# Kernel tuning notes

Hardware: AMD Instinct MI355X
Metric: run time of the kernel (lower is better)

## Reference

```python
import jax, jax.numpy as jnp
import numpy as np

MARGIN = 0.5          # triplet_margin
CLS_W = 1.0           # classification_weight
TRI_W = 1.0           # triplet_weight
SMOOTH = 0.1          # CrossEntropyLoss label_smoothing
PD_EPS = 1e-6         # torch pairwise_distance eps inside TripletMarginLoss


def setup_inputs() -> dict:
    key = jax.random.key(0)
    k1, k2, k3 = jax.random.split(key, 3)
    B, D, C = 8192, 128, 1000
    logits = jax.random.normal(k1, (B, C), dtype=jnp.float32)
    emb = jax.random.normal(k2, (B, D), dtype=jnp.float32)
    emb = emb / jnp.linalg.norm(emb, axis=1, keepdims=True)  # L2-normalized per docstring
    labels = jax.random.randint(k3, (B,), 0, C, dtype=jnp.int32)
    return {"logits": logits, "embeddings": emb, "labels": labels}


def _combined_loss(logits, embeddings, labels):
    # --- cross entropy with label smoothing 0.1 ---
    logp = jax.nn.log_softmax(logits, axis=-1)
    nll = -jnp.take_along_axis(logp, labels[:, None], axis=-1)[:, 0]
    smooth_term = -logp.mean(axis=-1)  # eps/C * sum(-logp) == eps * mean(-logp)
    cls_loss = ((1.0 - SMOOTH) * nll + SMOOTH * smooth_term).mean()

    # --- batch-hard triplet mining (vectorized over all rows) ---
    B = embeddings.shape[0]
    sq = jnp.sum(embeddings * embeddings, axis=1)
    # squared pairwise distances [B,B]; monotone in true distance, so ranking matches cdist
    d2 = sq[:, None] + sq[None, :] - 2.0 * (embeddings @ embeddings.T)
    eq = labels[:, None] == labels[None, :]
    pos_mask = eq & ~jnp.eye(B, dtype=bool)   # same class, not self
    neg_mask = ~eq
    big = jnp.finfo(d2.dtype).max
    hardest_pos = jnp.argmax(jnp.where(pos_mask, d2, -big), axis=1)  # farthest positive
    hardest_neg = jnp.argmin(jnp.where(neg_mask, d2, big), axis=1)   # closest negative
    valid = pos_mask.any(axis=1) & neg_mask.any(axis=1)

    # --- TripletMarginLoss(margin, p=2) over valid triplets ---
    a = embeddings
    p = embeddings[hardest_pos]
    n = embeddings[hardest_neg]
    d_ap = jnp.linalg.norm(a - p + PD_EPS, axis=1)  # torch adds eps inside the norm
    d_an = jnp.linalg.norm(a - n + PD_EPS, axis=1)
    per_row = jnp.maximum(d_ap - d_an + MARGIN, 0.0)
    cnt = jnp.sum(valid)
    triplet_loss = jnp.where(
        cnt > 0,
        jnp.sum(jnp.where(valid, per_row, 0.0)) / jnp.maximum(cnt, 1).astype(per_row.dtype),
        jnp.zeros((), per_row.dtype),
    )

    return CLS_W * cls_loss + TRI_W * triplet_loss


def reference(logits, embeddings, labels):
    return _combined_loss(logits, embeddings, labels)
```

## Files before the change

kernel.cpp:

```cpp
#include <hip/hip_runtime.h>

#define NB 8192
#define ND 128
#define NC 1000
#define NJC 16
#define JCB 4
#define JBS 128
#define NIS 32
#define CAP 64

typedef __attribute__((ext_vector_type(8))) short bf16x8;
typedef __attribute__((ext_vector_type(4))) float f32x4;

__device__ __forceinline__ unsigned short f2bf(float f) {
    unsigned int u = __float_as_uint(f);
    return (unsigned short)((u + 0x7fffu + ((u >> 16) & 1u)) >> 16);
}

__global__ __launch_bounds__(256) void ce_prep_kernel(const float* __restrict__ logits,
                                                      const float* __restrict__ emb,
                                                      const int* __restrict__ labels,
                                                      unsigned short* __restrict__ ebf,
                                                      float* __restrict__ cls_part,
                                                      int* __restrict__ cnt) {
    int wave = threadIdx.x >> 6, lane = threadIdx.x & 63;
    int r = blockIdx.x * 4 + wave;

    if (blockIdx.x == 0) {
        for (int k = threadIdx.x; k < NC; k += 256) cnt[k] = 0;
    }

    {
        const float* erow = emb + (size_t)r * ND;
        float2 v = *(const float2*)(erow + lane * 2);
        unsigned int packed = (unsigned int)f2bf(v.x) | ((unsigned int)f2bf(v.y) << 16);
        *(unsigned int*)(ebf + (size_t)r * ND + lane * 2) = packed;
    }

    const float* x = logits + (size_t)r * NC;
    float4 q0 = *(const float4*)(x + 4 * lane);
    float4 q1 = *(const float4*)(x + 256 + 4 * lane);
    float4 q2 = *(const float4*)(x + 512 + 4 * lane);
    float4 q3;
    bool a3 = (192 + lane) < 250;
    if (a3) q3 = *(const float4*)(x + 768 + 4 * lane);
    else q3 = make_float4(-3.4e38f, -3.4e38f, -3.4e38f, -3.4e38f);

    float m = fmaxf(fmaxf(fmaxf(q0.x, q0.y), fmaxf(q0.z, q0.w)),
                    fmaxf(fmaxf(q1.x, q1.y), fmaxf(q1.z, q1.w)));
    m = fmaxf(m, fmaxf(fmaxf(q2.x, q2.y), fmaxf(q2.z, q2.w)));
    m = fmaxf(m, fmaxf(fmaxf(q3.x, q3.y), fmaxf(q3.z, q3.w)));
    float s = (q0.x + q0.y + q0.z + q0.w) + (q1.x + q1.y + q1.z + q1.w) +
              (q2.x + q2.y + q2.z + q2.w) +
              (a3 ? (q3.x + q3.y + q3.z + q3.w) : 0.f);
#pragma unroll
    for (int o = 32; o >= 1; o >>= 1) {
        m = fmaxf(m, __shfl_xor(m, o));
        s += __shfl_xor(s, o);
    }
    float se = expf(q0.x - m) + expf(q0.y - m) + expf(q0.z - m) + expf(q0.w - m) +
               expf(q1.x - m) + expf(q1.y - m) + expf(q1.z - m) + expf(q1.w - m) +
               expf(q2.x - m) + expf(q2.y - m) + expf(q2.z - m) + expf(q2.w - m) +
               expf(q3.x - m) + expf(q3.y - m) + expf(q3.z - m) + expf(q3.w - m);
#pragma unroll
    for (int o = 32; o >= 1; o >>= 1) se += __shfl_xor(se, o);
    float xl = x[labels[r]];
    float v = (m + logf(se)) - 0.9f * xl - 0.1f * (s * (1.0f / NC));
    if (lane == 0) cls_part[r] = v;
}

__global__ __launch_bounds__(256) void bucket_kernel(const int* __restrict__ labels,
                                                     int* __restrict__ cnt,
                                                     int* __restrict__ lists) {
    int r = blockIdx.x * 256 + threadIdx.x;
    int c = labels[r];
    int slot = atomicAdd(&cnt[c], 1);
    if (slot < CAP) lists[c * CAP + slot] = r;
}

__global__ __launch_bounds__(256, 2) void mine_kernel(const unsigned short* __restrict__ ebf,
                                                      const int* __restrict__ labels,
                                                      float* __restrict__ part) {
    __shared__ unsigned short btile[2][JBS * ND];
    int tid = threadIdx.x;
    int wave = tid >> 6, lane = tid & 63;
    int col = lane & 15, grp = lane >> 4;
    int jchunk = blockIdx.x, jcbase = jchunk * (JCB * JBS);
    int ibase = blockIdx.y * 256 + wave * 64;

#define STAGE(buf, jb0)                                                                \
    do {                                                                               \
        _Pragma("unroll")                                                              \
        for (int rep = 0; rep < 8; ++rep) {                                            \
            int row = (tid >> 4) + rep * 16;                                           \
            const unsigned short* src =                                                \
                ebf + (size_t)((jb0) + row) * ND + (((tid & 15) ^ (row & 7)) << 3);    \
            unsigned short* dst = &btile[buf][0] + (size_t)(wave * 4 + rep * 16) * ND; \
            __builtin_amdgcn_global_load_lds(                                          \
                (const __attribute__((address_space(1))) unsigned int*)src,            \
                (__attribute__((address_space(3))) unsigned int*)dst, 16, 0, 0);       \
        }                                                                              \
    } while (0)

    STAGE(0, jcbase);

    bf16x8 af[4][4];
#pragma unroll
    for (int ic = 0; ic < 4; ++ic) {
        const unsigned short* ap = ebf + (size_t)(ibase + ic * 16 + col) * ND + (grp << 3);
#pragma unroll
        for (int kc = 0; kc < 4; ++kc) af[ic][kc] = *(const bf16x8*)(ap + kc * 32);
    }
    int li[16];
#pragma unroll
    for (int ic = 0; ic < 4; ++ic)
#pragma unroll
        for (int r = 0; r < 4; ++r) li[ic * 4 + r] = labels[ibase + ic * 16 + grp * 4 + r];
    int ljall[JCB * 8];
#pragma unroll
    for (int jb = 0; jb < JCB; ++jb)
#pragma unroll
        for (int st = 0; st < 8; ++st)
            ljall[jb * 8 + st] = labels[jcbase + jb * JBS + st * 16 + col];

    float bn[16];
#pragma unroll
    for (int k = 0; k < 16; ++k) bn[k] = -3.4e38f;

    __syncthreads();

#pragma unroll
    for (int t = 0; t < JCB; ++t) {
        if (t + 1 < JCB) STAGE((t + 1) & 1, jcbase + (t + 1) * JBS);

        const unsigned short* bt = &btile[t & 1][0];
#pragma unroll
        for (int st = 0; st < 8; ++st) {
            bf16x8 bfr[4];
#pragma unroll
            for (int kc = 0; kc < 4; ++kc) {
                int chunk = (grp + 4 * kc) ^ (col & 7);
                bfr[kc] = *(const bf16x8*)(bt + (size_t)(st * 16 + col) * ND + chunk * 8);
            }
            f32x4 acc[4] = {{0.f, 0.f, 0.f, 0.f}, {0.f, 0.f, 0.f, 0.f},
                            {0.f, 0.f, 0.f, 0.f}, {0.f, 0.f, 0.f, 0.f}};
#pragma unroll
            for (int kc = 0; kc < 4; ++kc)
#pragma unroll
                for (int ic = 0; ic < 4; ++ic)
                    acc[ic] = __builtin_amdgcn_mfma_f32_16x16x32_bf16(af[ic][kc], bfr[kc],
                                                                      acc[ic], 0, 0, 0);
            int lj = ljall[t * 8 + st];
#pragma unroll
            for (int ic = 0; ic < 4; ++ic)
#pragma unroll
                for (int r = 0; r < 4; ++r)
                    bn[ic * 4 + r] =
                        fmaxf(bn[ic * 4 + r], (lj == li[ic * 4 + r]) ? -3.4e38f : acc[ic][r]);
        }

        if (t + 1 < JCB) __syncthreads();
    }
#undef STAGE

#pragma unroll
    for (int k = 0; k < 16; ++k)
#pragma unroll
        for (int msk = 1; msk <= 8; msk <<= 1)
            bn[k] = fmaxf(bn[k], __shfl_xor(bn[k], msk));
    if (col == 0) {
#pragma unroll
        for (int ic = 0; ic < 4; ++ic)
#pragma unroll
            for (int r = 0; r < 4; ++r) {
                int gi = ibase + ic * 16 + grp * 4 + r;
                part[((size_t)gi << 4) + jchunk] = bn[ic * 4 + r];
            }
    }
}

__global__ __launch_bounds__(256) void reduce_kernel(const float* __restrict__ e,
                                                     const int* __restrict__ labels,
                                                     const float* __restrict__ part,
                                                     const int* __restrict__ cnt,
                                                     const int* __restrict__ lists,
                                                     float2* __restrict__ tri_part) {
    int wave = threadIdx.x >> 6, lane = threadIdx.x & 63;
    int r = blockIdx.x * 4 + wave;
    int g = lane >> 3, sl = lane & 7;

    float nb = part[((size_t)r << 4) + (lane & 15)];
#pragma unroll
    for (int o = 1; o <= 8; o <<= 1) nb = fmaxf(nb, __shfl_xor(nb, o));
    float d_an = sqrtf(fmaxf(2.0f - 2.0f * nb, 0.0f));

    int myl = labels[r];
    int ctot = cnt[myl];
    int n = min(ctot, CAP);
    const float* a = e + (size_t)r * ND;

    float4 a0 = *(const float4*)(a + sl * 16);
    float4 a1 = *(const float4*)(a + sl * 16 + 4);
    float4 a2 = *(const float4*)(a + sl * 16 + 8);
    float4 a3 = *(const float4*)(a + sl * 16 + 12);

    float best = -1.0f;
    int jp = r;
    for (int base = 0; base < n; base += 8) {
        int idx = base + g;
        bool ok = (idx < n);
        int j2 = ok ? lists[myl * CAP + idx] : r;
        const float* p = e + (size_t)j2 * ND;
        float4 p0 = *(const float4*)(p + sl * 16);
        float4 p1 = *(const float4*)(p + sl * 16 + 4);
        float4 p2 = *(const float4*)(p + sl * 16 + 8);
        float4 p3 = *(const float4*)(p + sl * 16 + 12);
        float d, ss = 0.f;
        d = a0.x - p0.x; ss += d * d; d = a0.y - p0.y; ss += d * d;
        d = a0.z - p0.z; ss += d * d; d = a0.w - p0.w; ss += d * d;
        d = a1.x - p1.x; ss += d * d; d = a1.y - p1.y; ss += d * d;
        d = a1.z - p1.z; ss += d * d; d = a1.w - p1.w; ss += d * d;
        d = a2.x - p2.x; ss += d * d; d = a2.y - p2.y; ss += d * d;
        d = a2.z - p2.z; ss += d * d; d = a2.w - p2.w; ss += d * d;
        d = a3.x - p3.x; ss += d * d; d = a3.y - p3.y; ss += d * d;
        d = a3.z - p3.z; ss += d * d; d = a3.w - p3.w; ss += d * d;
        ss += __shfl_xor(ss, 1);
        ss += __shfl_xor(ss, 2);
        ss += __shfl_xor(ss, 4);
        float d2v = (ok && j2 != r) ? ss : -2.0f;
        if (d2v > best || (d2v == best && j2 < jp)) { best = d2v; jp = j2; }
    }
#pragma unroll
    for (int msk = 8; msk <= 32; msk <<= 1) {
        float ob = __shfl_xor(best, msk);
        int oj = __shfl_xor(jp, msk);
        if (ob > best || (ob == best && oj < jp)) { best = ob; jp = oj; }
    }
    bool valid = (ctot >= 2) && (ctot < NB);

    const float* p = e + (size_t)jp * ND;
    float2 av = *(const float2*)(a + lane * 2);
    float2 pv = *(const float2*)(p + lane * 2);
    float dx = av.x - pv.x + 1e-6f, dy = av.y - pv.y + 1e-6f;
    float ss = dx * dx + dy * dy;
#pragma unroll
    for (int o = 32; o >= 1; o >>= 1) ss += __shfl_xor(ss, o);
    float d_ap = sqrtf(ss);

    if (lane == 0) {
        float per = valid ? fmaxf(d_ap - d_an + 0.5f, 0.0f) : 0.0f;
        tri_part[r] = make_float2(per, valid ? 1.0f : 0.0f);
    }
}

__global__ __launch_bounds__(1024) void fin_kernel(const float* __restrict__ cls_part,
                                                   const float2* __restrict__ tri_part,
                                                   float* __restrict__ out) {
    __shared__ float sc[16], sp[16], sn[16];
    int t = threadIdx.x;
    int wave = t >> 6, lane = t & 63;
    float c = 0.f, tp = 0.f, tc = 0.f;
    for (int k = t; k < NB; k += 1024) {
        c += cls_part[k];
        float2 q = tri_part[k];
        tp += q.x;
        tc += q.y;
    }
#pragma unroll
    for (int o = 32; o >= 1; o >>= 1) {
        c += __shfl_xor(c, o);
        tp += __shfl_xor(tp, o);
        tc += __shfl_xor(tc, o);
    }
    if (lane == 0) { sc[wave] = c; sp[wave] = tp; sn[wave] = tc; }
    __syncthreads();
    if (t == 0) {
        float C = 0.f, P = 0.f, V = 0.f;
        for (int w = 0; w < 16; ++w) { C += sc[w]; P += sp[w]; V += sn[w]; }
        float cls = C * (1.0f / NB);
        float tri = V > 0.5f ? P / V : 0.0f;
        out[0] = cls + tri;
    }
}

extern "C" void kernel_launch(void* const* d_in, const int* in_sizes, int n_in,
                              void* d_out, int out_size, void* d_ws, size_t ws_size,
                              hipStream_t stream) {
    const float* logits = (const float*)d_in[0];
    const float* emb = (const float*)d_in[1];
    const int* labels = (const int*)d_in[2];

    char* w = (char*)d_ws;
    unsigned short* ebf = (unsigned short*)w;
    float* part = (float*)(w + 2097152);
    float* cls_part = (float*)(w + 2621440);
    float2* tri_part = (float2*)(w + 2654208);
    int* cnt = (int*)(w + 2719744);
    int* lists = (int*)(w + 2723840);

    ce_prep_kernel<<<NB / 4, 256, 0, stream>>>(logits, emb, labels, ebf, cls_part, cnt);
    bucket_kernel<<<NB / 256, 256, 0, stream>>>(labels, cnt, lists);
    mine_kernel<<<dim3(NJC, NIS), 256, 0, stream>>>(ebf, labels, part);
    reduce_kernel<<<NB / 4, 256, 0, stream>>>(emb, labels, part, cnt, lists, tri_part);
    fin_kernel<<<1, 1024, 0, stream>>>(cls_part, tri_part, (float*)d_out);
}
```

Before: 50.97 us.

## Widen mining blocks to 512 threads and pre-reduce triplet partials per block

After: 50.41 us. About the same (-1.1%).

```diff
diff --git a/kernel.cpp b/kernel.cpp
--- a/kernel.cpp
+++ b/kernel.cpp
@@ -6,8 +6,9 @@
 #define NJC 16
 #define JCB 4
 #define JBS 128
-#define NIS 32
+#define NIS 16
 #define CAP 64
+#define NRB (NB / 4)
 
 typedef __attribute__((ext_vector_type(8))) short bf16x8;
 typedef __attribute__((ext_vector_type(4))) float f32x4;
@@ -78,7 +79,7 @@
     if (slot < CAP) lists[c * CAP + slot] = r;
 }
 
-__global__ __launch_bounds__(256, 2) void mine_kernel(const unsigned short* __restrict__ ebf,
+__global__ __launch_bounds__(512, 2) void mine_kernel(const unsigned short* __restrict__ ebf,
                                                       const int* __restrict__ labels,
                                                       float* __restrict__ part) {
     __shared__ unsigned short btile[2][JBS * ND];
@@ -86,20 +87,21 @@
     int wave = tid >> 6, lane = tid & 63;
     int col = lane & 15, grp = lane >> 4;
     int jchunk = blockIdx.x, jcbase = jchunk * (JCB * JBS);
-    int ibase = blockIdx.y * 256 + wave * 64;
-
-#define STAGE(buf, jb0)                                                                \
-    do {                                                                               \
-        _Pragma("unroll")                                                              \
-        for (int rep = 0; rep < 8; ++rep) {                                            \
-            int row = (tid >> 4) + rep * 16;                                           \
-            const unsigned short* src =                                                \
-                ebf + (size_t)((jb0) + row) * ND + (((tid & 15) ^ (row & 7)) << 3);    \
-            unsigned short* dst = &btile[buf][0] + (size_t)(wave * 4 + rep * 16) * ND; \
-            __builtin_amdgcn_global_load_lds(                                          \
-                (const __attribute__((address_space(1))) unsigned int*)src,            \
-                (__attribute__((address_space(3))) unsigned int*)dst, 16, 0, 0);       \
-        }                                                                              \
+    int ibase = blockIdx.y * 512 + wave * 64;
+
+#define STAGE(buf, jb0)                                                                 \
+    do {                                                                                \
+        _Pragma("unroll")                                                               \
+        for (int rep = 0; rep < 4; ++rep) {                                             \
+            int row = (tid >> 4) + rep * 32;                                            \
+            const unsigned short* src =                                                 \
+                ebf + (size_t)((jb0) + row) * ND + (((tid & 15) ^ (row & 7)) << 3);     \
+            unsigned short* dst =                                                       \
+                &btile[buf][0] + (size_t)((tid >> 6) * 4 + rep * 32) * ND;              \
+            __builtin_amdgcn_global_load_lds(                                           \
+                (const __attribute__((address_space(1))) unsigned int*)src,             \
+                (__attribute__((address_space(3))) unsigned int*)dst, 16, 0, 0);        \
+        }                                                                               \
     } while (0)
 
     STAGE(0, jcbase);
@@ -184,7 +186,9 @@
                                                      const float* __restrict__ part,
                                                      const int* __restrict__ cnt,
                                                      const int* __restrict__ lists,
-                                                     float2* __restrict__ tri_part) {
+                                                     const float* __restrict__ cls_part,
+                                                     float4* __restrict__ blk) {
+    __shared__ float sp[4], sv[4], sc[4];
     int wave = threadIdx.x >> 6, lane = threadIdx.x & 63;
     int r = blockIdx.x * 4 + wave;
     int g = lane >> 3, sl = lane & 7;
@@ -248,38 +252,42 @@
     float d_ap = sqrtf(ss);
 
     if (lane == 0) {
-        float per = valid ? fmaxf(d_ap - d_an + 0.5f, 0.0f) : 0.0f;
-        tri_part[r] = make_float2(per, valid ? 1.0f : 0.0f);
-    }
-}
-
-__global__ __launch_bounds__(1024) void fin_kernel(const float* __restrict__ cls_part,
-                                                   const float2* __restrict__ tri_part,
+        sp[wave] = valid ? fmaxf(d_ap - d_an + 0.5f, 0.0f) : 0.0f;
+        sv[wave] = valid ? 1.0f : 0.0f;
+        sc[wave] = cls_part[r];
+    }
+    __syncthreads();
+    if (threadIdx.x == 0)
+        blk[blockIdx.x] = make_float4(sp[0] + sp[1] + sp[2] + sp[3],
+                                      sv[0] + sv[1] + sv[2] + sv[3],
+                                      sc[0] + sc[1] + sc[2] + sc[3], 0.f);
+}
+
+__global__ __launch_bounds__(1024) void fin_kernel(const float4* __restrict__ blk,
                                                    float* __restrict__ out) {
     __shared__ float sc[16], sp[16], sn[16];
     int t = threadIdx.x;
     int wave = t >> 6, lane = t & 63;
-    float c = 0.f, tp = 0.f, tc = 0.f;
-    for (int k = t; k < NB; k += 1024) {
-        c += cls_part[k];
-        float2 q = tri_part[k];
+    float tp = 0.f, tv = 0.f, c = 0.f;
+    for (int k = t; k < NRB; k += 1024) {
+        float4 q = blk[k];
         tp += q.x;
-        tc += q.y;
+        tv += q.y;
+        c += q.z;
     }
 #pragma unroll
     for (int o = 32; o >= 1; o >>= 1) {
+        tp += __shfl_xor(tp, o);
+        tv += __shfl_xor(tv, o);
         c += __shfl_xor(c, o);
-        tp += __shfl_xor(tp, o);
-        tc += __shfl_xor(tc, o);
-    }
-    if (lane == 0) { sc[wave] = c; sp[wave] = tp; sn[wave] = tc; }
+    }
+    if (lane == 0) { sp[wave] = tp; sn[wave] = tv; sc[wave] = c; }
     __syncthreads();
     if (t == 0) {
-        float C = 0.f, P = 0.f, V = 0.f;
-        for (int w = 0; w < 16; ++w) { C += sc[w]; P += sp[w]; V += sn[w]; }
-        float cls = C * (1.0f / NB);
+        float P = 0.f, V = 0.f, C = 0.f;
+        for (int w = 0; w < 16; ++w) { P += sp[w]; V += sn[w]; C += sc[w]; }
         float tri = V > 0.5f ? P / V : 0.0f;
-        out[0] = cls + tri;
+        out[0] = C * (1.0f / NB) + tri;
     }
 }
 
@@ -294,13 +302,13 @@
     unsigned short* ebf = (unsigned short*)w;
     float* part = (float*)(w + 2097152);
     float* cls_part = (float*)(w + 2621440);
-    float2* tri_part = (float2*)(w + 2654208);
-    int* cnt = (int*)(w + 2719744);
-    int* lists = (int*)(w + 2723840);
+    int* cnt = (int*)(w + 2654208);
+    int* lists = (int*)(w + 2658304);
+    float4* blk = (float4*)(w + 2920448);
 
     ce_prep_kernel<<<NB / 4, 256, 0, stream>>>(logits, emb, labels, ebf, cls_part, cnt);
     bucket_kernel<<<NB / 256, 256, 0, stream>>>(labels, cnt, lists);
-    mine_kernel<<<dim3(NJC, NIS), 256, 0, stream>>>(ebf, labels, part);
-    reduce_kernel<<<NB / 4, 256, 0, stream>>>(emb, labels, part, cnt, lists, tri_part);
-    fin_kernel<<<1, 1024, 0, stream>>>(cls_part, tri_part, (float*)d_out);
-}
+    mine_kernel<<<dim3(NJC, NIS), 512, 0, stream>>>(ebf, labels, part);
+    reduce_kernel<<<NRB, 256, 0, stream>>>(emb, labels, part, cnt, lists, cls_part, blk);
+    fin_kernel<<<1, 1024, 0, stream>>>(blk, (float*)d_out);
+}
```
